# Performance work log

Hardware: AMD Instinct MI355X
Metric: run time of the kernel (lower is better)

The kernel has to match this reference:

```python
import jax, jax.numpy as jnp
import numpy as np

B, IN, HID, OUT, E, C, TOPK = 4096, 1024, 2048, 1024, 8, 1000, 2
EPS = 1e-6


def setup_inputs() -> dict:
    key = jax.random.key(0)
    ks = jax.random.split(key, 8)
    def xavier(k, fan_out, fan_in):
        lim = float(np.sqrt(6.0 / (fan_in + fan_out)))
        return jax.random.uniform(k, (fan_out, fan_in), jnp.float32, -lim, lim)
    return {
        "x": jax.random.normal(ks[0], (B, IN), jnp.float32),
        "Wg": xavier(ks[1], E, IN),
        "bg": jnp.zeros((E,), jnp.float32),
        "gamma": jnp.ones((1, E), jnp.float32),
        "beta": jnp.zeros((1, E), jnp.float32),
        "W1": xavier(ks[2], HID * E, IN),
        "b1": jnp.zeros((HID * E,), jnp.float32),
        "W2": xavier(ks[3], OUT * E, HID * E),
        "b2": jnp.zeros((OUT * E,), jnp.float32),
        "Wc": xavier(ks[4], C, OUT),
        "bc": jnp.zeros((C,), jnp.float32),
    }


def reference(x, Wg, bg, gamma, beta, W1, b1, W2, b2, Wc, bc):
    # gating (noise_std=0 -> no noise)
    gate_logits = x @ Wg.T + bg                      # [B, E]
    # GRN over expert dim
    Gx = jnp.linalg.norm(gate_logits, axis=1, keepdims=True)   # [B, 1]
    Nx = Gx / (jnp.mean(Gx, axis=0, keepdims=True) + EPS)      # [B, 1]
    gate_logits = gamma * (gate_logits * Nx) + beta
    gate_probs = jax.nn.softmax(gate_logits, axis=-1)
    topk_probs, topk_idx = jax.lax.top_k(gate_probs, TOPK)     # [B, K]
    # dense all-expert MLP (fc2 mixes across ALL experts' hidden units, as in source)
    h = jax.nn.relu(x @ W1.T + b1)                   # [B, HID*E]
    eo = (h @ W2.T + b2).reshape(B, E, OUT)          # [B, E, OUT]
    sel = jnp.take_along_axis(eo, topk_idx[:, :, None], axis=1)  # [B, K, OUT]
    out = jnp.einsum('bk,bkd->bd', topk_probs, sel)  # [B, OUT]
    return out @ Wc.T + bc                           # [B, C]
```

## Files before the change

### kernel.cpp

```cpp
#include <hip/hip_runtime.h>
#include <stdint.h>

#define B_SZ   4096
#define IN_SZ  1024
#define NE     8
#define NC     1000
#define HIDE   16384
#define OUTE   1024
#define GEPS   1e-6f
#define NSPLIT 2
#define KSPL   8192

typedef __attribute__((ext_vector_type(8))) short short8;
typedef __attribute__((ext_vector_type(4))) float floatx4;

__device__ __forceinline__ unsigned short f2bf(float f) {
    unsigned u = __float_as_uint(f);
    u += 0x7fffu + ((u >> 16) & 1u);
    return (unsigned short)(u >> 16);
}
__device__ __forceinline__ float bf2f(unsigned short h) {
    return __uint_as_float(((unsigned)h) << 16);
}

__device__ __forceinline__ void async16(const void* g, void* l) {
    __builtin_amdgcn_global_load_lds(
        (const __attribute__((address_space(1))) void*)g,
        (__attribute__((address_space(3))) void*)l, 16, 0, 0);
}

__device__ __forceinline__ void cvt_span(const float* __restrict__ src,
                                         unsigned short* __restrict__ dst,
                                         int n, int bid, int nb) {
    int i = (bid * 256 + (int)threadIdx.x) * 8;
    int stride = nb * 256 * 8;
    for (; i < n; i += stride) {
        float4 v0 = *(const float4*)(src + i);
        float4 v1 = *(const float4*)(src + i + 4);
        uint4 w;
        w.x = (unsigned)f2bf(v0.x) | ((unsigned)f2bf(v0.y) << 16);
        w.y = (unsigned)f2bf(v0.z) | ((unsigned)f2bf(v0.w) << 16);
        w.z = (unsigned)f2bf(v1.x) | ((unsigned)f2bf(v1.y) << 16);
        w.w = (unsigned)f2bf(v1.z) | ((unsigned)f2bf(v1.w) << 16);
        *(uint4*)(dst + i) = w;
    }
}

__global__ __launch_bounds__(256) void k_gatef(const float* __restrict__ x,
                                               const float* __restrict__ Wg,
                                               const float* __restrict__ bg,
                                               float* __restrict__ logits,
                                               float* __restrict__ Gx,
                                               unsigned short* __restrict__ xb,
                                               const float* __restrict__ W1,
                                               unsigned short* __restrict__ w1b,
                                               const float* __restrict__ Wc,
                                               unsigned short* __restrict__ wcb) {
    const int bid = blockIdx.x;
    if (bid >= 1024) {
        if (bid < 1536) cvt_span(W1, w1b, HIDE * IN_SZ, bid - 1024, 512);
        else            cvt_span(Wc, wcb, NC * IN_SZ,   bid - 1536, 64);
        return;
    }
    int wid = threadIdx.x >> 6, lane = threadIdx.x & 63;
    int b = bid * 4 + wid;
    const float* xr = x + (size_t)b * IN_SZ;
    float xv[16];
#pragma unroll
    for (int t = 0; t < 16; ++t) xv[t] = xr[lane + 64 * t];
    unsigned short* xbr = xb + (size_t)b * IN_SZ;
#pragma unroll
    for (int t = 0; t < 16; ++t) xbr[lane + 64 * t] = f2bf(xv[t]);
    float lg[NE];
#pragma unroll
    for (int e = 0; e < NE; ++e) {
        const float* wr = Wg + e * IN_SZ;
        float s = 0.f;
#pragma unroll
        for (int t = 0; t < 16; ++t) s += xv[t] * wr[lane + 64 * t];
#pragma unroll
        for (int m = 32; m >= 1; m >>= 1) s += __shfl_xor(s, m, 64);
        lg[e] = s + bg[e];
    }
    if (lane == 0) {
        float ss = 0.f;
#pragma unroll
        for (int e = 0; e < NE; ++e) { logits[b * NE + e] = lg[e]; ss += lg[e] * lg[e]; }
        Gx[b] = sqrtf(ss);
    }
}

__global__ __launch_bounds__(1024) void k_gsum(const float* __restrict__ Gx,
                                               float* __restrict__ gsum, int* __restrict__ ctrl) {
    __shared__ float sm[1024];
    int t = threadIdx.x;
    if (t < 24) ctrl[t] = 0;
    sm[t] = Gx[t] + Gx[t + 1024] + Gx[t + 2048] + Gx[t + 3072];
    __syncthreads();
    for (int m = 512; m >= 1; m >>= 1) {
        if (t < m) sm[t] += sm[t + m];
        __syncthreads();
    }
    if (t == 0) gsum[0] = sm[0];
}

__global__ __launch_bounds__(256) void k_topk(const float* __restrict__ logits,
                                              const float* __restrict__ Gx,
                                              const float* __restrict__ gsum,
                                              const float* __restrict__ gamma,
                                              const float* __restrict__ beta,
                                              int* __restrict__ tidx, float* __restrict__ tp,
                                              int* __restrict__ counts) {
    int b = blockIdx.x * 256 + threadIdx.x;
    float nx = Gx[b] / (gsum[0] * (1.0f / (float)B_SZ) + GEPS);
    float l[NE];
    float mx = -1e30f;
#pragma unroll
    for (int e = 0; e < NE; ++e) {
        l[e] = gamma[e] * (logits[b * NE + e] * nx) + beta[e];
        mx = fmaxf(mx, l[e]);
    }
    float se = 0.f;
#pragma unroll
    for (int e = 0; e < NE; ++e) { l[e] = expf(l[e] - mx); se += l[e]; }
    float inv = 1.f / se;
    int i0 = 0; float p0 = l[0];
#pragma unroll
    for (int e = 1; e < NE; ++e) if (l[e] > p0) { p0 = l[e]; i0 = e; }
    int i1 = -1; float p1 = -1.f;
#pragma unroll
    for (int e = 0; e < NE; ++e) if (e != i0 && l[e] > p1) { p1 = l[e]; i1 = e; }
    tidx[b * 2 + 0] = i0; tidx[b * 2 + 1] = i1;
    tp[b * 2 + 0] = p0 * inv; tp[b * 2 + 1] = p1 * inv;
    atomicAdd(&counts[i0], 1);
    atomicAdd(&counts[i1], 1);
}

__global__ void k_offsets(const int* __restrict__ counts, int* __restrict__ offs) {
    if (threadIdx.x == 0) {
        int a = 0;
        for (int e = 0; e < NE; ++e) { offs[e] = a; a += counts[e]; }
    }
}

__global__ __launch_bounds__(256) void k_fill(const int* __restrict__ tidx, const float* __restrict__ tp,
                                              const int* __restrict__ offs, int* __restrict__ cursors,
                                              int* __restrict__ rowsw, int* __restrict__ slotof) {
    int b = blockIdx.x * 256 + threadIdx.x;
#pragma unroll
    for (int k = 0; k < 2; ++k) {
        int e = tidx[b * 2 + k];
        int pos = atomicAdd(&cursors[e], 1);
        int at = offs[e] + pos;
        rowsw[at] = b * 2 + k;
        slotof[b * 2 + k] = at;
    }
}


__device__ __forceinline__ void compute_bk64(const short* buf, const int* aoff, const int* boff,
                                             floatx4 acc[4][4]) {
    const short* sA = buf;
    const short* sB = buf + 8192;
    short8 a0[4], a1[4], b0[4], b1[4];
#pragma unroll
    for (int i = 0; i < 4; ++i) {
        a0[i] = *(const short8*)(sA + aoff[i]);
        a1[i] = *(const short8*)(sA + (aoff[i] ^ 32));
        b0[i] = *(const short8*)(sB + boff[i]);
        b1[i] = *(const short8*)(sB + (boff[i] ^ 32));
    }
    asm volatile("s_waitcnt lgkmcnt(0)" ::: "memory");
    __builtin_amdgcn_sched_barrier(0);
    __builtin_amdgcn_s_setprio(1);
#pragma unroll
    for (int i = 0; i < 4; ++i)
#pragma unroll
        for (int j = 0; j < 4; ++j) {
            acc[i][j] = __builtin_amdgcn_mfma_f32_16x16x32_bf16(a0[i], b0[j], acc[i][j], 0, 0, 0);
            acc[i][j] = __builtin_amdgcn_mfma_f32_16x16x32_bf16(a1[i], b1[j], acc[i][j], 0, 0, 0);
        }
    __builtin_amdgcn_s_setprio(0);
}

__device__ __forceinline__ void stage_bk64(const unsigned short* const* pa,
                                           const unsigned short* const* pb,
                                           char* bufc, int koff, int tid) {
#pragma unroll
    for (int c = 0; c < 4; ++c) {
        async16(pa[c] + koff, bufc + c * 4096 + tid * 16);
        async16(pb[c] + koff, bufc + 16384 + c * 4096 + tid * 16);
    }
}

__device__ __forceinline__ void core64db(const unsigned short* const* pa,
                                         const unsigned short* const* pb,
                                         short* smem, int nkt, int wm, int wn,
                                         int tid, int lane, floatx4 acc[4][4]) {
    char* b0c = (char*)smem;
    char* b1c = b0c + 32768;
    const int sl = ((lane >> 4) ^ (lane & 7)) * 8;
    int aoff[4], boff[4];
#pragma unroll
    for (int i = 0; i < 4; ++i) {
        aoff[i] = (wm * 64 + i * 16 + (lane & 15)) * 64 + sl;
        boff[i] = (wn * 64 + i * 16 + (lane & 15)) * 64 + sl;
    }
    stage_bk64(pa, pb, b0c, 0, tid);
    __syncthreads();
#pragma unroll 1
    for (int kt = 0; kt < nkt; kt += 2) {
        if (kt + 1 < nkt) stage_bk64(pa, pb, b1c, (kt + 1) * 64, tid);
        compute_bk64(smem, aoff, boff, acc);
        __syncthreads();
        if (kt + 2 < nkt) stage_bk64(pa, pb, b0c, (kt + 2) * 64, tid);
        compute_bk64(smem + 16384, aoff, boff, acc);
        __syncthreads();
    }
}

__global__ __launch_bounds__(256) void k_h8f(const unsigned short* __restrict__ xb,
                                             const unsigned short* __restrict__ w1b,
                                             const float* __restrict__ b1,
                                             unsigned short* __restrict__ hout,
                                             const float* __restrict__ W2,
                                             unsigned short* __restrict__ w2b) {
    const int bid = blockIdx.x;
    const int role = bid % 5;
    if (role == 4) {
        cvt_span(W2, w2b, NE * OUTE * HIDE, bid / 5, 1024);
        return;
    }
    const int hbid = (bid / 5) * 4 + role;
    extern __shared__ short smem[];
    const int tid = threadIdx.x, lane = tid & 63, wid = tid >> 6;
    const int wm = wid >> 1, wn = wid & 1;
    const int wg = (hbid & 7) * 512 + (hbid >> 3);
    const int mt = wg & 31, nt = wg >> 5;
    const int m0 = mt * 128, n0 = nt * 128;
    const int srow = tid >> 3;
    const int cswz = ((tid & 7) ^ (srow & 7)) * 8;
    const unsigned short* pa[4];
    const unsigned short* pb[4];
#pragma unroll
    for (int c = 0; c < 4; ++c) {
        pa[c] = xb  + (size_t)(m0 + 32 * c + srow) * IN_SZ + cswz;
        pb[c] = w1b + (size_t)(n0 + 32 * c + srow) * IN_SZ + cswz;
    }
    floatx4 acc[4][4] = {};
    core64db(pa, pb, smem, IN_SZ / 64, wm, wn, tid, lane, acc);
#pragma unroll
    for (int i = 0; i < 4; ++i)
#pragma unroll
        for (int j = 0; j < 4; ++j)
#pragma unroll
            for (int r = 0; r < 4; ++r) {
                int row = m0 + wm * 64 + i * 16 + (lane >> 4) * 4 + r;
                int col = n0 + wn * 64 + j * 16 + (lane & 15);
                float v = acc[i][j][r] + b1[col];
                hout[(size_t)row * HIDE + col] = f2bf(fmaxf(v, 0.f));
            }
}

__global__ __launch_bounds__(256) void k_moe(const unsigned short* __restrict__ h,
                                             const unsigned short* __restrict__ w2b,
                                             const int* __restrict__ counts,
                                             const int* __restrict__ offs,
                                             const int* __restrict__ rowsw,
                                             unsigned short* __restrict__ parts) {
    const int wg = (blockIdx.x & 7) * (gridDim.x >> 3) + (blockIdx.x >> 3);
    const int mt = wg & 31, nt = (wg >> 5) & 7, sp = (wg >> 8) & 1, e = wg >> 9;
    const int gn = counts[e];
    if (mt * 128 >= gn) return;
    const int gbase = offs[e];
    extern __shared__ short smem[];
    const int tid = threadIdx.x, lane = tid & 63, wid = tid >> 6;
    const int wm = wid >> 1, wn = wid & 1;
    const int srow = tid >> 3;
    const int cswz = ((tid & 7) ^ (srow & 7)) * 8;
    const unsigned short* pa[4];
    const unsigned short* pb[4];
#pragma unroll
    for (int c = 0; c < 4; ++c) {
        int lr = mt * 128 + 32 * c + srow;
        if (lr > gn - 1) lr = gn - 1;
        int grow = rowsw[gbase + lr] >> 1;
        pa[c] = h + (size_t)grow * HIDE + sp * KSPL + cswz;
        pb[c] = w2b + (size_t)(e * OUTE + nt * 128 + 32 * c + srow) * HIDE + sp * KSPL + cswz;
    }
    floatx4 acc[4][4] = {};
    core64db(pa, pb, smem, KSPL / 64, wm, wn, tid, lane, acc);
    unsigned short* pbase = parts + (size_t)sp * B_SZ * 2 * OUTE;
#pragma unroll
    for (int i = 0; i < 4; ++i)
#pragma unroll
        for (int j = 0; j < 4; ++j)
#pragma unroll
            for (int r = 0; r < 4; ++r) {
                int lr = mt * 128 + wm * 64 + i * 16 + (lane >> 4) * 4 + r;
                if (lr < gn) {
                    int at = gbase + lr;
                    int col = nt * 128 + wn * 64 + j * 16 + (lane & 15);
                    pbase[(size_t)at * OUTE + col] = f2bf(acc[i][j][r]);
                }
            }
}

__global__ __launch_bounds__(256) void k_reduce(const unsigned short* __restrict__ parts,
                                                const int* __restrict__ slotof,
                                                const int* __restrict__ tidx,
                                                const float* __restrict__ tp,
                                                const float* __restrict__ b2,
                                                unsigned short* __restrict__ ymix) {
    int i = blockIdx.x * 256 + threadIdx.x;
    int b = i >> 8, col = (i & 255) * 4;
    int at0 = slotof[b * 2], at1 = slotof[b * 2 + 1];
    int e0 = tidx[b * 2], e1 = tidx[b * 2 + 1];
    float q0 = tp[b * 2], q1 = tp[b * 2 + 1];
    float y0[4] = {0.f, 0.f, 0.f, 0.f}, y1[4] = {0.f, 0.f, 0.f, 0.f};
#pragma unroll
    for (int sp = 0; sp < NSPLIT; ++sp) {
        ushort4 u0 = *(const ushort4*)(parts + ((size_t)sp * B_SZ * 2 + at0) * OUTE + col);
        ushort4 u1 = *(const ushort4*)(parts + ((size_t)sp * B_SZ * 2 + at1) * OUTE + col);
        y0[0] += bf2f(u0.x); y0[1] += bf2f(u0.y); y0[2] += bf2f(u0.z); y0[3] += bf2f(u0.w);
        y1[0] += bf2f(u1.x); y1[1] += bf2f(u1.y); y1[2] += bf2f(u1.z); y1[3] += bf2f(u1.w);
    }
    float4 bb0 = *(const float4*)(b2 + (size_t)e0 * OUTE + col);
    float4 bb1 = *(const float4*)(b2 + (size_t)e1 * OUTE + col);
    ushort4 o;
    o.x = f2bf(q0 * (y0[0] + bb0.x) + q1 * (y1[0] + bb1.x));
    o.y = f2bf(q0 * (y0[1] + bb0.y) + q1 * (y1[1] + bb1.y));
    o.z = f2bf(q0 * (y0[2] + bb0.z) + q1 * (y1[2] + bb1.z));
    o.w = f2bf(q0 * (y0[3] + bb0.w) + q1 * (y1[3] + bb1.w));
    *(ushort4*)(ymix + (size_t)b * OUTE + col) = o;
}

__global__ __launch_bounds__(256) void k_gemm_out(const unsigned short* __restrict__ ymix,
                                                  const unsigned short* __restrict__ wcb,
                                                  const float* __restrict__ bc,
                                                  float* __restrict__ out) {
    const int mt = blockIdx.x >> 3, nt = blockIdx.x & 7;
    const int m0 = mt * 128, n0 = nt * 128;
    extern __shared__ short smem[];
    const int tid = threadIdx.x, lane = tid & 63, wid = tid >> 6;
    const int wm = wid >> 1, wn = wid & 1;
    const int srow = tid >> 3;
    const int cswz = ((tid & 7) ^ (srow & 7)) * 8;
    const unsigned short* pa[4];
    const unsigned short* pb[4];
#pragma unroll
    for (int c = 0; c < 4; ++c) {
        pa[c] = ymix + (size_t)(m0 + 32 * c + srow) * IN_SZ + cswz;
        int br = n0 + 32 * c + srow; if (br > NC - 1) br = NC - 1;
        pb[c] = wcb + (size_t)br * IN_SZ + cswz;
    }
    floatx4 acc[4][4] = {};
    core64db(pa, pb, smem, IN_SZ / 64, wm, wn, tid, lane, acc);
#pragma unroll
    for (int i = 0; i < 4; ++i)
#pragma unroll
        for (int j = 0; j < 4; ++j)
#pragma unroll
            for (int r = 0; r < 4; ++r) {
                int row = m0 + wm * 64 + i * 16 + (lane >> 4) * 4 + r;
                int col = n0 + wn * 64 + j * 16 + (lane & 15);
                if (col < NC)
                    out[(size_t)row * NC + col] = acc[i][j][r] + bc[col];
            }
}

extern "C" void kernel_launch(void* const* d_in, const int* in_sizes, int n_in,
                              void* d_out, int out_size, void* d_ws, size_t ws_size,
                              hipStream_t stream) {
    const float* x     = (const float*)d_in[0];
    const float* Wg    = (const float*)d_in[1];
    const float* bg    = (const float*)d_in[2];
    const float* gamma = (const float*)d_in[3];
    const float* beta  = (const float*)d_in[4];
    const float* W1    = (const float*)d_in[5];
    const float* b1    = (const float*)d_in[6];
    const float* W2    = (const float*)d_in[7];
    const float* b2    = (const float*)d_in[8];
    const float* Wc    = (const float*)d_in[9];
    const float* bc    = (const float*)d_in[10];
    float* out = (float*)d_out;

    char* ws = (char*)d_ws;
    size_t o = 0;
    auto carve = [&](size_t bytes) { char* p = ws + o; o += (bytes + 255) & ~(size_t)255; return p; };
    unsigned short* xb    = (unsigned short*)carve((size_t)B_SZ * IN_SZ * 2);
    unsigned short* w1b   = (unsigned short*)carve((size_t)HIDE * IN_SZ * 2);
    unsigned short* w2b   = (unsigned short*)carve((size_t)NE * OUTE * HIDE * 2);
    unsigned short* wcb   = (unsigned short*)carve((size_t)NC * IN_SZ * 2);
    unsigned short* h     = (unsigned short*)carve((size_t)B_SZ * HIDE * 2);
    unsigned short* parts = (unsigned short*)carve((size_t)NSPLIT * B_SZ * 2 * OUTE * 2);
    unsigned short* ymix  = (unsigned short*)carve((size_t)B_SZ * OUTE * 2);
    float* logits = (float*)carve((size_t)B_SZ * NE * 4);
    float* Gx     = (float*)carve((size_t)B_SZ * 4);
    int*   tidx   = (int*)carve((size_t)B_SZ * 2 * 4);
    float* tp     = (float*)carve((size_t)B_SZ * 2 * 4);
    int*   rowsw  = (int*)carve((size_t)B_SZ * 2 * 4);
    int*   slotof = (int*)carve((size_t)B_SZ * 2 * 4);
    int*   ctrl   = (int*)carve(256);
    int* counts  = ctrl;
    int* cursors = ctrl + 8;
    int* offs    = ctrl + 16;
    float* gsum  = (float*)(ctrl + 24);

    hipFuncSetAttribute((const void*)k_h8f,      hipFuncAttributeMaxDynamicSharedMemorySize, 65536);
    hipFuncSetAttribute((const void*)k_moe,      hipFuncAttributeMaxDynamicSharedMemorySize, 65536);
    hipFuncSetAttribute((const void*)k_gemm_out, hipFuncAttributeMaxDynamicSharedMemorySize, 65536);

    k_gatef<<<1600, 256, 0, stream>>>(x, Wg, bg, logits, Gx, xb, W1, w1b, Wc, wcb);
    k_gsum<<<1, 1024, 0, stream>>>(Gx, gsum, ctrl);
    k_topk<<<B_SZ / 256, 256, 0, stream>>>(logits, Gx, gsum, gamma, beta, tidx, tp, counts);
    k_offsets<<<1, 64, 0, stream>>>(counts, offs);
    k_fill<<<B_SZ / 256, 256, 0, stream>>>(tidx, tp, offs, cursors, rowsw, slotof);

    k_h8f<<<5120, 256, 65536, stream>>>(xb, w1b, b1, h, W2, w2b);
    k_moe<<<NE * 32 * 8 * NSPLIT, 256, 65536, stream>>>(h, w2b, counts, offs, rowsw, parts);
    k_reduce<<<B_SZ, 256, 0, stream>>>(parts, slotof, tidx, tp, b2, ymix);
    k_gemm_out<<<(B_SZ / 128) * 8, 256, 65536, stream>>>(ymix, wcb, bc, out);
}
```

Baseline: 898.2 us.

## Spread W2 bf16 conversion across gating kernels instead of fc1 GEMM

The fp32-to-bf16 conversion of the large W2 matrix is moved out of the fc1 GEMM kernel, where it occupied every fifth block. It is split into five chunks, each appended as extra blocks to one of the small gating, gsum, top-k, offsets and fill kernels. The fc1 GEMM becomes a pure GEMM with a grid-derived tile swizzle. The aim is to hide the memory-bound conversion behind the latency-bound small kernels, which leave most of the device idle. The cost is that those serial gating kernels now carry heavy bandwidth work and may lengthen the critical path, while the fc1 GEMM no longer overlaps any conversion.

New measurement: 881.5 us. No clear change (-1.9%).

```diff
diff --git a/kernel.cpp b/kernel.cpp
--- a/kernel.cpp
+++ b/kernel.cpp
@@ -11,6 +11,13 @@
 #define NSPLIT 2
 #define KSPL   8192
 
+#define W2TOT  134217728
+#define SA     33554432
+#define SB     41943040
+#define SC     25165824
+#define SD     12582912
+#define SE     20971520
+
 typedef __attribute__((ext_vector_type(8))) short short8;
 typedef __attribute__((ext_vector_type(4))) float floatx4;
 
@@ -32,8 +39,9 @@
 __device__ __forceinline__ void cvt_span(const float* __restrict__ src,
                                          unsigned short* __restrict__ dst,
                                          int n, int bid, int nb) {
-    int i = (bid * 256 + (int)threadIdx.x) * 8;
-    int stride = nb * 256 * 8;
+    const int bdim = (int)blockDim.x;
+    int i = (bid * bdim + (int)threadIdx.x) * 8;
+    int stride = nb * bdim * 8;
     for (; i < n; i += stride) {
         float4 v0 = *(const float4*)(src + i);
         float4 v1 = *(const float4*)(src + i + 4);
@@ -55,11 +63,14 @@
                                                const float* __restrict__ W1,
                                                unsigned short* __restrict__ w1b,
                                                const float* __restrict__ Wc,
-                                               unsigned short* __restrict__ wcb) {
+                                               unsigned short* __restrict__ wcb,
+                                               const float* __restrict__ W2,
+                                               unsigned short* __restrict__ w2b) {
     const int bid = blockIdx.x;
     if (bid >= 1024) {
-        if (bid < 1536) cvt_span(W1, w1b, HIDE * IN_SZ, bid - 1024, 512);
-        else            cvt_span(Wc, wcb, NC * IN_SZ,   bid - 1536, 64);
+        if (bid < 1536)      cvt_span(W1, w1b, HIDE * IN_SZ, bid - 1024, 512);
+        else if (bid < 1600) cvt_span(Wc, wcb, NC * IN_SZ,   bid - 1536, 64);
+        else                 cvt_span(W2, w2b, SA,           bid - 1600, 1024);
         return;
     }
     int wid = threadIdx.x >> 6, lane = threadIdx.x & 63;
@@ -90,8 +101,14 @@
     }
 }
 
-__global__ __launch_bounds__(1024) void k_gsum(const float* __restrict__ Gx,
-                                               float* __restrict__ gsum, int* __restrict__ ctrl) {
+__global__ __launch_bounds__(1024) void k_gsumf(const float* __restrict__ Gx,
+                                                float* __restrict__ gsum, int* __restrict__ ctrl,
+                                                const float* __restrict__ W2,
+                                                unsigned short* __restrict__ w2b) {
+    if (blockIdx.x > 0) {
+        cvt_span(W2 + SA, w2b + SA, SB, blockIdx.x - 1, 2047);
+        return;
+    }
     __shared__ float sm[1024];
     int t = threadIdx.x;
     if (t < 24) ctrl[t] = 0;
@@ -104,13 +121,19 @@
     if (t == 0) gsum[0] = sm[0];
 }
 
-__global__ __launch_bounds__(256) void k_topk(const float* __restrict__ logits,
-                                              const float* __restrict__ Gx,
-                                              const float* __restrict__ gsum,
-                                              const float* __restrict__ gamma,
-                                              const float* __restrict__ beta,
-                                              int* __restrict__ tidx, float* __restrict__ tp,
-                                              int* __restrict__ counts) {
+__global__ __launch_bounds__(256) void k_topkf(const float* __restrict__ logits,
+                                               const float* __restrict__ Gx,
+                                               const float* __restrict__ gsum,
+                                               const float* __restrict__ gamma,
+                                               const float* __restrict__ beta,
+                                               int* __restrict__ tidx, float* __restrict__ tp,
+                                               int* __restrict__ counts,
+                                               const float* __restrict__ W2,
+                                               unsigned short* __restrict__ w2b) {
+    if (blockIdx.x >= 16) {
+        cvt_span(W2 + (SA + SB), w2b + (SA + SB), SC, blockIdx.x - 16, 1024);
+        return;
+    }
     int b = blockIdx.x * 256 + threadIdx.x;
     float nx = Gx[b] / (gsum[0] * (1.0f / (float)B_SZ) + GEPS);
     float l[NE];
@@ -136,16 +159,29 @@
     atomicAdd(&counts[i1], 1);
 }
 
-__global__ void k_offsets(const int* __restrict__ counts, int* __restrict__ offs) {
+__global__ __launch_bounds__(256) void k_offsetsf(const int* __restrict__ counts,
+                                                  int* __restrict__ offs,
+                                                  const float* __restrict__ W2,
+                                                  unsigned short* __restrict__ w2b) {
+    if (blockIdx.x > 0) {
+        cvt_span(W2 + (SA + SB + SC), w2b + (SA + SB + SC), SD, blockIdx.x - 1, 511);
+        return;
+    }
     if (threadIdx.x == 0) {
         int a = 0;
         for (int e = 0; e < NE; ++e) { offs[e] = a; a += counts[e]; }
     }
 }
 
-__global__ __launch_bounds__(256) void k_fill(const int* __restrict__ tidx, const float* __restrict__ tp,
-                                              const int* __restrict__ offs, int* __restrict__ cursors,
-                                              int* __restrict__ rowsw, int* __restrict__ slotof) {
+__global__ __launch_bounds__(256) void k_fillf(const int* __restrict__ tidx, const float* __restrict__ tp,
+                                               const int* __restrict__ offs, int* __restrict__ cursors,
+                                               int* __restrict__ rowsw, int* __restrict__ slotof,
+                                               const float* __restrict__ W2,
+                                               unsigned short* __restrict__ w2b) {
+    if (blockIdx.x >= 16) {
+        cvt_span(W2 + (SA + SB + SC + SD), w2b + (SA + SB + SC + SD), SE, blockIdx.x - 16, 1008);
+        return;
+    }
     int b = blockIdx.x * 256 + threadIdx.x;
 #pragma unroll
     for (int k = 0; k < 2; ++k) {
@@ -219,23 +255,14 @@
     }
 }
 
-__global__ __launch_bounds__(256) void k_h8f(const unsigned short* __restrict__ xb,
-                                             const unsigned short* __restrict__ w1b,
-                                             const float* __restrict__ b1,
-                                             unsigned short* __restrict__ hout,
-                                             const float* __restrict__ W2,
-                                             unsigned short* __restrict__ w2b) {
-    const int bid = blockIdx.x;
-    const int role = bid % 5;
-    if (role == 4) {
-        cvt_span(W2, w2b, NE * OUTE * HIDE, bid / 5, 1024);
-        return;
-    }
-    const int hbid = (bid / 5) * 4 + role;
+__global__ __launch_bounds__(256) void k_h8(const unsigned short* __restrict__ xb,
+                                            const unsigned short* __restrict__ w1b,
+                                            const float* __restrict__ b1,
+                                            unsigned short* __restrict__ hout) {
     extern __shared__ short smem[];
     const int tid = threadIdx.x, lane = tid & 63, wid = tid >> 6;
     const int wm = wid >> 1, wn = wid & 1;
-    const int wg = (hbid & 7) * 512 + (hbid >> 3);
+    const int wg = (blockIdx.x & 7) * (gridDim.x >> 3) + (blockIdx.x >> 3);
     const int mt = wg & 31, nt = wg >> 5;
     const int m0 = mt * 128, n0 = nt * 128;
     const int srow = tid >> 3;
@@ -407,17 +434,17 @@
     int* offs    = ctrl + 16;
     float* gsum  = (float*)(ctrl + 24);
 
-    hipFuncSetAttribute((const void*)k_h8f,      hipFuncAttributeMaxDynamicSharedMemorySize, 65536);
+    hipFuncSetAttribute((const void*)k_h8,       hipFuncAttributeMaxDynamicSharedMemorySize, 65536);
     hipFuncSetAttribute((const void*)k_moe,      hipFuncAttributeMaxDynamicSharedMemorySize, 65536);
     hipFuncSetAttribute((const void*)k_gemm_out, hipFuncAttributeMaxDynamicSharedMemorySize, 65536);
 
-    k_gatef<<<1600, 256, 0, stream>>>(x, Wg, bg, logits, Gx, xb, W1, w1b, Wc, wcb);
-    k_gsum<<<1, 1024, 0, stream>>>(Gx, gsum, ctrl);
-    k_topk<<<B_SZ / 256, 256, 0, stream>>>(logits, Gx, gsum, gamma, beta, tidx, tp, counts);
-    k_offsets<<<1, 64, 0, stream>>>(counts, offs);
-    k_fill<<<B_SZ / 256, 256, 0, stream>>>(tidx, tp, offs, cursors, rowsw, slotof);
-
-    k_h8f<<<5120, 256, 65536, stream>>>(xb, w1b, b1, h, W2, w2b);
+    k_gatef<<<2624, 256, 0, stream>>>(x, Wg, bg, logits, Gx, xb, W1, w1b, Wc, wcb, W2, w2b);
+    k_gsumf<<<2048, 1024, 0, stream>>>(Gx, gsum, ctrl, W2, w2b);
+    k_topkf<<<1040, 256, 0, stream>>>(logits, Gx, gsum, gamma, beta, tidx, tp, counts, W2, w2b);
+    k_offsetsf<<<512, 256, 0, stream>>>(counts, offs, W2, w2b);
+    k_fillf<<<1024, 256, 0, stream>>>(tidx, tp, offs, cursors, rowsw, slotof, W2, w2b);
+
+    k_h8<<<(B_SZ / 128) * (HIDE / 128), 256, 65536, stream>>>(xb, w1b, b1, h);
     k_moe<<<NE * 32 * 8 * NSPLIT, 256, 65536, stream>>>(h, w2b, counts, offs, rowsw, parts);
     k_reduce<<<B_SZ, 256, 0, stream>>>(parts, slotof, tidx, tp, b2, ymix);
     k_gemm_out<<<(B_SZ / 128) * 8, 256, 65536, stream>>>(ymix, wcb, bc, out);
```
